# Kernel tuning notes

Measured on AMD Instinct MI355X. Metric: run time of the kernel, lower is better.

Reference implementation:

```python
import jax, jax.numpy as jnp
import numpy as np

N = 100000          # nodes
E = 800000          # edges per relation
R = 6               # relations
B = 1000            # graphs
IN_DIM = 14
POS_COL = 5
PE = 8              # pos_emb_dim
H = 128             # hidden_dim
OUT = 128           # out_dim
NPOS = 24
D1 = IN_DIM - 1 + PE  # 21, GAT layer-1 input dim


def setup_inputs() -> dict:
    key = jax.random.key(0)
    ks = jax.random.split(key, 20)
    x_all = jax.random.normal(ks[0], (N, IN_DIM), dtype=jnp.float32)
    pos = jax.random.randint(ks[1], (N,), 0, NPOS)
    x_all = x_all.at[:, POS_COL].set(pos.astype(jnp.float32))
    edges = jax.random.randint(ks[2], (R, 2, E), 0, N, dtype=jnp.int32)
    batch = jnp.sort(jax.random.randint(ks[3], (N,), 0, B, dtype=jnp.int32))
    pos_table = jax.random.normal(ks[4], (NPOS, PE), dtype=jnp.float32) * 0.02
    W1 = jax.random.normal(ks[5], (R, D1, H), dtype=jnp.float32) * 0.1
    as1 = jax.random.normal(ks[6], (R, H), dtype=jnp.float32) * 0.1
    ad1 = jax.random.normal(ks[7], (R, H), dtype=jnp.float32) * 0.1
    b1 = jnp.zeros((R, H), dtype=jnp.float32)
    W2 = jax.random.normal(ks[8], (R, H, H), dtype=jnp.float32) * 0.05
    as2 = jax.random.normal(ks[9], (R, H), dtype=jnp.float32) * 0.1
    ad2 = jax.random.normal(ks[10], (R, H), dtype=jnp.float32) * 0.1
    b2 = jnp.zeros((R, H), dtype=jnp.float32)
    n1w = jnp.ones((H,), dtype=jnp.float32)
    n1b = jnp.zeros((H,), dtype=jnp.float32)
    n2w = jnp.ones((H,), dtype=jnp.float32)
    n2b = jnp.zeros((H,), dtype=jnp.float32)
    query = jax.random.normal(ks[11], (H,), dtype=jnp.float32) * 0.02
    projW = jax.random.normal(ks[12], (H, OUT), dtype=jnp.float32) * 0.05
    projb = jnp.zeros((OUT,), dtype=jnp.float32)
    return dict(x_all=x_all, edges=edges, batch=batch, pos_table=pos_table,
                W1=W1, as1=as1, ad1=ad1, b1=b1, W2=W2, as2=as2, ad2=ad2, b2=b2,
                n1w=n1w, n1b=n1b, n2w=n2w, n2b=n2b, query=query, projW=projW, projb=projb)


def _seg_softmax(logits, seg, num):
    m = jax.lax.stop_gradient(jax.ops.segment_max(logits, seg, num_segments=num))
    e = jnp.exp(logits - m[seg])
    s = jax.ops.segment_sum(e, seg, num_segments=num)
    return e / s[seg]


def _gat_layer(x, W, a_s, a_d, b, edges):
    # sum over R relation-specific GATConv(heads=1, concat=False) outputs
    n = x.shape[0]
    out = jnp.zeros((n, W.shape[-1]), dtype=x.dtype)
    for r in range(R):
        xp = x @ W[r]                       # [N, H] projected features
        src, dst = edges[r, 0], edges[r, 1]
        z = (xp @ a_s[r])[src] + (xp @ a_d[r])[dst]
        z = jnp.where(z > 0, z, 0.2 * z)    # LeakyReLU(0.2)
        alpha = _seg_softmax(z, dst, n)     # per-destination softmax
        agg = jax.ops.segment_sum(alpha[:, None] * xp[src], dst, num_segments=n)
        out = out + agg + b[r]
    return out


def _ln(x, w, b):
    mu = x.mean(-1, keepdims=True)
    v = ((x - mu) ** 2).mean(-1, keepdims=True)
    return (x - mu) / jnp.sqrt(v + 1e-5) * w + b


def reference(x_all, edges, batch, pos_table, W1, as1, ad1, b1,
              W2, as2, ad2, b2, n1w, n1b, n2w, n2b, query, projW, projb):
    cont = jnp.concatenate([x_all[:, :POS_COL], x_all[:, POS_COL + 1:]], axis=1)
    pidx = jnp.clip(x_all[:, POS_COL].astype(jnp.int32), 0, NPOS - 1)
    x = jnp.concatenate([cont, pos_table[pidx]], axis=1)  # [N, D1]
    x = _gat_layer(x, W1, as1, ad1, b1, edges)
    x = _ln(jax.nn.gelu(x, approximate=False), n1w, n1b)
    x = _gat_layer(x, W2, as2, ad2, b2, edges)
    x = _ln(jax.nn.gelu(x, approximate=False), n2w, n2b)
    # AttentionPooling: gather-score-softmax-scatter over batch segments
    scores = x @ query
    w = _seg_softmax(scores, batch, B)
    pool = jax.ops.segment_sum(w[:, None] * x, batch, num_segments=B)  # [B, H]
    return pool @ projW + projb
```

## Files before the change

### kernel.cpp

```cpp
#include <hip/hip_runtime.h>
#include <math.h>

#define NN   100000
#define EE   800000
#define RR   6
#define BB   1000
#define HH   128
#define MM   (RR*NN)
#define NBPR ((NN + 255) >> 8)
#define NBK  (RR * NBPR)
#define CH   4096
#define CAP  4096

static inline int ceil_div(int a, int b){ return (a+b-1)/b; }

typedef __attribute__((ext_vector_type(8))) short bf16x8;
typedef __attribute__((ext_vector_type(4))) short bf16x4;
typedef __attribute__((ext_vector_type(4))) float f32x4;

__device__ __forceinline__ unsigned fenc(float f){
  unsigned u = __float_as_uint(f);
  return (u & 0x80000000u) ? ~u : (u | 0x80000000u);
}
__device__ __forceinline__ float fdec(unsigned u){
  return __uint_as_float((u & 0x80000000u) ? (u & 0x7fffffffu) : ~u);
}
__device__ __forceinline__ unsigned short f2bf(float f){
  unsigned u = __float_as_uint(f);
  return (unsigned short)((u + 0x7fffu + ((u >> 16) & 1u)) >> 16);
}
__device__ __forceinline__ float bf2f(unsigned short h){
  return __uint_as_float(((unsigned)h) << 16);
}

__global__ void k_binscatter(const int* __restrict__ edges, int* __restrict__ bcur,
                             unsigned* __restrict__ ebkt)
{
  __shared__ int hist[NBPR];
  __shared__ int base[NBPR];
  int t = threadIdx.x;
  const int nch = (EE + CH - 1) / CH;
  int r = blockIdx.x / nch, c = blockIdx.x - r*nch;
  for (int i = t; i < NBPR; i += 256) hist[i] = 0;
  __syncthreads();
  const int* sptr = edges + (size_t)r*2*EE;
  const int* dptr = sptr + EE;
  int e0 = c*CH, e1 = min(EE, e0 + CH);
  for (int i = e0 + t; i < e1; i += 256)
    atomicAdd(&hist[dptr[i] >> 8], 1);
  __syncthreads();
  for (int i = t; i < NBPR; i += 256) {
    int h = hist[i];
    int gb = r*NBPR + i;
    base[i] = h ? (gb*CAP + atomicAdd(&bcur[gb], h)) : 0;
    hist[i] = 0;
  }
  __syncthreads();
  for (int i = e0 + t; i < e1; i += 256) {
    int dst = dptr[i];
    int b = dst >> 8;
    int slot = base[b] + atomicAdd(&hist[b], 1);
    ebkt[slot] = ((unsigned)sptr[i] << 8) | (unsigned)(dst & 255);
  }
}

__global__ void k_bscan(const int* __restrict__ bcur, int* __restrict__ boff,
                        int* __restrict__ off)
{
  __shared__ int sh[256];
  int t = threadIdx.x;
  int carry = 0;
  for (int c = 0; c < NBK; c += 256) {
    int idx = c + t;
    int v = (idx < NBK) ? bcur[idx] : 0;
    sh[t] = v;
    __syncthreads();
    for (int o = 1; o < 256; o <<= 1) {
      int add = (t >= o) ? sh[t-o] : 0;
      __syncthreads();
      sh[t] += add;
      __syncthreads();
    }
    int incl = sh[t];
    int tot  = sh[255];
    if (idx < NBK) boff[idx] = carry + incl - v;
    __syncthreads();
    carry += tot;
  }
  if (t == 0) { boff[NBK] = carry; off[MM] = carry; }
}

__global__ void k_bbuild(const unsigned* __restrict__ ebkt, const int* __restrict__ bcur,
                         const int* __restrict__ boff,
                         int* __restrict__ off, int* __restrict__ elist)
{
  __shared__ int cnt[256];
  __shared__ int sc[256];
  __shared__ int cur[256];
  int t = threadIdx.x;
  int bb = blockIdx.x;
  int e0r = bb*CAP, e1r = e0r + bcur[bb];
  int w0 = boff[bb];
  cnt[t] = 0;
  __syncthreads();
  for (int i = e0r + t; i < e1r; i += 256)
    atomicAdd(&cnt[ebkt[i] & 255u], 1);
  __syncthreads();
  sc[t] = cnt[t];
  __syncthreads();
  for (int o = 1; o < 256; o <<= 1) {
    int add = (t >= o) ? sc[t-o] : 0;
    __syncthreads();
    sc[t] += add;
    __syncthreads();
  }
  int excl = sc[t] - cnt[t];
  int r = bb / NBPR, b = bb - r*NBPR;
  int dst = b*256 + t;
  if (dst < NN) off[r*NN + dst] = w0 + excl;
  cur[t] = w0 + excl;
  __syncthreads();
  for (int i = e0r + t; i < e1r; i += 256) {
    unsigned w = ebkt[i];
    int slot = atomicAdd(&cur[w & 255u], 1);
    elist[slot] = (int)(w >> 8);
  }
}

__global__ void k_featprep(const float* __restrict__ x_all, const float* __restrict__ pos_table,
                           short* __restrict__ x0h, short* __restrict__ x0l)
{
  int gid = blockIdx.x*256 + threadIdx.x;
  if (gid >= NN*32) return;
  int nidx = gid >> 5, c = gid & 31;
  float v = 0.f;
  if (c < 13) {
    int scl = (c < 5) ? c : c + 1;
    v = x_all[nidx*14 + scl];
  } else if (c < 21) {
    int pi = (int)x_all[nidx*14 + 5];
    pi = pi < 0 ? 0 : (pi > 23 ? 23 : pi);
    v = pos_table[pi*8 + (c - 13)];
  }
  unsigned short h = f2bf(v);
  unsigned short l = f2bf(v - bf2f(h));
  x0h[gid] = (short)h;
  x0l[gid] = (short)l;
}

template<int KP>
__global__ void k_wprep(const float* __restrict__ W, int K,
                        short* __restrict__ Wh, short* __restrict__ Wl)
{
  int gid = blockIdx.x*256 + threadIdx.x;
  if (gid >= RR*128*KP) return;
  int r = gid / (128*KP);
  int rem = gid - r*(128*KP);
  int nn = rem / KP, k = rem - nn*KP;
  float v = (k < K) ? W[((size_t)r*K + k)*128 + nn] : 0.f;
  unsigned short h = f2bf(v);
  unsigned short l = f2bf(v - bf2f(h));
  Wh[gid] = (short)h;
  Wl[gid] = (short)l;
}

template<int KP>
__global__ void k_wa(const float* __restrict__ W, const float* __restrict__ as,
                     const float* __restrict__ ad, int K, float* __restrict__ wa)
{
  int idx = blockIdx.x*256 + threadIdx.x;
  if (idx >= 12*KP) return;
  int rr = idx / KP, k = idx - rr*KP;
  int r = (rr < 6) ? rr : rr - 6;
  const float* a = ((rr < 6) ? as : ad) + (size_t)r*HH;
  float s = 0.f;
  if (k < K) {
    const float* wrow = W + ((size_t)r*K + k)*128;
    #pragma unroll 8
    for (int h = 0; h < 128; ++h) s = fmaf(wrow[h], a[h], s);
  }
  wa[idx] = s;
}

__global__ void k_zsd32(const short* __restrict__ xh, const short* __restrict__ xl,
                        const float* __restrict__ wa, float* __restrict__ zsd, int n)
{
  __shared__ float w[12*32];
  int tid = threadIdx.x;
  for (int i = tid; i < 12*32; i += 256) w[i] = wa[i];
  __syncthreads();
  int g = blockIdx.x*256 + tid;
  if (g >= n) return;
  float v[32];
  #pragma unroll
  for (int c = 0; c < 4; ++c) {
    uint4 vh = *(const uint4*)(xh + (size_t)g*32 + c*8);
    uint4 vl = *(const uint4*)(xl + (size_t)g*32 + c*8);
    const unsigned short* hp = (const unsigned short*)&vh;
    const unsigned short* lp = (const unsigned short*)&vl;
    #pragma unroll
    for (int j = 0; j < 8; ++j) v[c*8+j] = bf2f(hp[j]) + bf2f(lp[j]);
  }
  #pragma unroll
  for (int rr = 0; rr < 12; ++rr) {
    float d = 0.f;
    #pragma unroll
    for (int k = 0; k < 32; ++k) d = fmaf(v[k], w[rr*32+k], d);
    zsd[(size_t)rr*n + g] = d;
  }
}

__global__ void k_agg1(const unsigned short* __restrict__ x0h, const float* __restrict__ zsd,
                       const int* __restrict__ elist, const int* __restrict__ off,
                       unsigned short* __restrict__ aggH, unsigned short* __restrict__ aggL,
                       int n)
{
  int gid = blockIdx.x*256 + threadIdx.x;
  int g = gid >> 4;
  int l = threadIdx.x & 15;
  if (g >= n) return;
  int sub = l >> 2, ch = l & 3;

  for (int rel = 0; rel < RR; ++rel) {
    const float* zsr = zsd + (size_t)rel*n;
    const float* zdr = zsd + (size_t)(6+rel)*n;
    int o0 = off[(size_t)rel*NN + g];
    int deg = off[(size_t)rel*NN + g + 1] - o0;
    float acc[8] = {0,0,0,0,0,0,0,0};
    float inv = 0.f;
    if (deg > 0) {
      float zdd = zdr[g];
      float m = -3.4e38f, es = 0.f;
      for (int i = l; i < deg; i += 16) {
        float z = zsr[elist[o0+i]] + zdd;
        z = (z > 0.f) ? z : 0.2f*z;
        float mn = fmaxf(m, z);
        es = es*__expf(m - mn) + __expf(z - mn);
        m = mn;
      }
      #pragma unroll
      for (int o = 1; o <= 8; o <<= 1) {
        float mo = __shfl_xor(m, o), eo = __shfl_xor(es, o);
        float mn = fmaxf(m, mo);
        es = es*__expf(m - mn) + eo*__expf(mo - mn);
        m = mn;
      }
      inv = 1.f / es;
      for (int base = 0; base < deg; base += 4) {
        int i = base + sub;
        float ew = 0.f; int ss = 0;
        if (i < deg) {
          ss = elist[o0+i];
          float z = zsr[ss] + zdd;
          z = (z > 0.f) ? z : 0.2f*z;
          ew = __expf(z - m);
        }
        uint4 v = *(const uint4*)(x0h + (size_t)ss*32 + ch*8);
        acc[0] = fmaf(ew, __uint_as_float(v.x << 16),         acc[0]);
        acc[1] = fmaf(ew, __uint_as_float(v.x & 0xffff0000u), acc[1]);
        acc[2] = fmaf(ew, __uint_as_float(v.y << 16),         acc[2]);
        acc[3] = fmaf(ew, __uint_as_float(v.y & 0xffff0000u), acc[3]);
        acc[4] = fmaf(ew, __uint_as_float(v.z << 16),         acc[4]);
        acc[5] = fmaf(ew, __uint_as_float(v.z & 0xffff0000u), acc[5]);
        acc[6] = fmaf(ew, __uint_as_float(v.w << 16),         acc[6]);
        acc[7] = fmaf(ew, __uint_as_float(v.w & 0xffff0000u), acc[7]);
      }
      #pragma unroll
      for (int j = 0; j < 8; ++j) {
        acc[j] += __shfl_xor(acc[j], 4);
        acc[j] += __shfl_xor(acc[j], 8);
      }
    }
    if (sub == 0) {
      uint4 ph, pl;
      unsigned* php = (unsigned*)&ph; unsigned* plp = (unsigned*)&pl;
      #pragma unroll
      for (int j2 = 0; j2 < 4; ++j2) {
        float a0 = acc[2*j2]   * inv;
        float a1 = acc[2*j2+1] * inv;
        unsigned short h0 = f2bf(a0), h1 = f2bf(a1);
        php[j2] = ((unsigned)h1 << 16) | h0;
        plp[j2] = ((unsigned)f2bf(a1 - bf2f(h1)) << 16) | f2bf(a0 - bf2f(h0));
      }
      size_t o = ((size_t)rel*n + g)*32 + ch*8;
      *(uint4*)(aggH + o) = ph;
      *(uint4*)(aggL + o) = pl;
    }
  }
}

__device__ __forceinline__ bf16x8 ldfragG(const short* __restrict__ p, int row, int kb, int KP_)
{
  bf16x4 a = *(const bf16x4*)(p + (size_t)row*KP_ + kb);
  bf16x4 b = *(const bf16x4*)(p + (size_t)row*KP_ + kb + 16);
  return __builtin_shufflevector(a, b, 0,1,2,3,4,5,6,7);
}

__global__ __launch_bounds__(256, 4)
void k_gemm1(const short* __restrict__ aggH, const short* __restrict__ aggL,
             const short* __restrict__ Wh, const short* __restrict__ Wl,
             const float* __restrict__ bsv,
             const float* __restrict__ nw, const float* __restrict__ nb,
             unsigned short* __restrict__ Yh, unsigned short* __restrict__ Yl, int n)
{
  __shared__ __align__(16) float Cs[32*136];
  int tid = threadIdx.x;
  int r0 = blockIdx.x * 32;
  int wid = tid >> 6, lane = tid & 63;
  int lr = lane & 15, lg = lane >> 4;
  int rt = wid >> 1;
  int c0 = (wid & 1) * 4;
  int arow = r0 + rt*16 + lr;
  int kb = 4*lg;
  f32x4 acct[4] = {{0,0,0,0},{0,0,0,0},{0,0,0,0},{0,0,0,0}};

  for (int rel = 0; rel < RR; ++rel) {
    const short* Ahr = aggH + (size_t)rel*n*32;
    const short* Alr = aggL + (size_t)rel*n*32;
    const short* Whr = Wh + (size_t)rel*128*32;
    const short* Wlr = Wl + (size_t)rel*128*32;
    bf16x8 ah = ldfragG(Ahr, arow, kb, 32);
    bf16x8 al = ldfragG(Alr, arow, kb, 32);
    #pragma unroll
    for (int t = 0; t < 4; ++t) {
      int wrow = (c0 + t)*16 + lr;
      bf16x8 whf = ldfragG(Whr, wrow, kb, 32);
      bf16x8 wlf = ldfragG(Wlr, wrow, kb, 32);
      acct[t] = __builtin_amdgcn_mfma_f32_16x16x32_bf16(ah, whf, acct[t], 0, 0, 0);
      acct[t] = __builtin_amdgcn_mfma_f32_16x16x32_bf16(al, whf, acct[t], 0, 0, 0);
      acct[t] = __builtin_amdgcn_mfma_f32_16x16x32_bf16(ah, wlf, acct[t], 0, 0, 0);
    }
  }

  #pragma unroll
  for (int t = 0; t < 4; ++t)
    #pragma unroll
    for (int v = 0; v < 4; ++v) {
      int row = rt*16 + lg*4 + v;
      int col = (c0 + t)*16 + lr;
      float x = acct[t][v] + bsv[col];
      Cs[row*136 + col] = 0.5f*x*(1.f + erff(x*0.70710678118654752f));
    }
  __syncthreads();
  {
    int r = tid >> 3, sg = tid & 7;
    float vals[16];
    float s = 0.f;
    #pragma unroll
    for (int i = 0; i < 16; ++i) { vals[i] = Cs[r*136 + sg*16 + i]; s += vals[i]; }
    s += __shfl_xor(s, 1); s += __shfl_xor(s, 2); s += __shfl_xor(s, 4);
    float mu = s * (1.f/128.f);
    float var = 0.f;
    #pragma unroll
    for (int i = 0; i < 16; ++i) { vals[i] -= mu; var += vals[i]*vals[i]; }
    var += __shfl_xor(var, 1); var += __shfl_xor(var, 2); var += __shfl_xor(var, 4);
    float inv = 1.f / sqrtf(var*(1.f/128.f) + 1e-5f);
    int g = r0 + r;
    uint4 ph0, ph1, pl0, pl1;
    unsigned* php0 = (unsigned*)&ph0; unsigned* php1 = (unsigned*)&ph1;
    unsigned* plp0 = (unsigned*)&pl0; unsigned* plp1 = (unsigned*)&pl1;
    #pragma unroll
    for (int j2 = 0; j2 < 8; ++j2) {
      int c = sg*16 + 2*j2;
      float y0 = vals[2*j2]  *inv*nw[c]   + nb[c];
      float y1 = vals[2*j2+1]*inv*nw[c+1] + nb[c+1];
      unsigned short h0 = f2bf(y0), h1 = f2bf(y1);
      unsigned hw = ((unsigned)h1 << 16) | h0;
      unsigned lw = ((unsigned)f2bf(y1 - bf2f(h1)) << 16) | f2bf(y0 - bf2f(h0));
      if (j2 < 4) { php0[j2] = hw; plp0[j2] = lw; }
      else        { php1[j2-4] = hw; plp1[j2-4] = lw; }
    }
    *(uint4*)(Yh + (size_t)g*128 + sg*16)     = ph0;
    *(uint4*)(Yh + (size_t)g*128 + sg*16 + 8) = ph1;
    *(uint4*)(Yl + (size_t)g*128 + sg*16)     = pl0;
    *(uint4*)(Yl + (size_t)g*128 + sg*16 + 8) = pl1;
  }
}

__device__ __forceinline__ bf16x8 ldfrag_(const short* p, int row, int kb, int KP_, int smask)
{
  int xr = row & smask;
  int s0 = (((kb)      >> 3) ^ xr) * 8 + (kb & 7);
  int s1 = (((kb + 16) >> 3) ^ xr) * 8 + (kb & 7);
  bf16x4 a = *(const bf16x4*)(p + (size_t)row*KP_ + s0);
  bf16x4 b = *(const bf16x4*)(p + (size_t)row*KP_ + s1);
  return __builtin_shufflevector(a, b, 0,1,2,3,4,5,6,7);
}

template<int KP>
__global__ __launch_bounds__(256, 2)
void k_gemm_mfma(const short* __restrict__ Ah, const short* __restrict__ Al,
                 const short* __restrict__ WhAll, const short* __restrict__ WlAll,
                 const float* __restrict__ a_sAll, const float* __restrict__ a_dAll,
                 unsigned short* __restrict__ xpbAll, float* __restrict__ zsAll,
                 float* __restrict__ zdAll, int rbase, int n)
{
  constexpr int SLOTS = KP/8;
  constexpr int SMASK = (SLOTS >= 8) ? 7 : (SLOTS-1);
  __shared__ short lds[320*KP];
  constexpr int AH0 = 0, AL0 = 32*KP, WH0 = 64*KP, WL0 = 192*KP;
  int tid = threadIdx.x;
  int r0 = blockIdx.x * 32;
  int ry = blockIdx.y;
  const short* Wh = WhAll + (size_t)(rbase+ry)*128*KP;
  const short* Wl = WlAll + (size_t)(rbase+ry)*128*KP;
  const float* a_s = a_sAll + (size_t)(rbase+ry)*HH;
  const float* a_d = a_dAll + (size_t)(rbase+ry)*HH;
  unsigned short* xpb = xpbAll + (size_t)ry*n*128;
  float* zs = zsAll + (size_t)ry*n;
  float* zd = zdAll + (size_t)ry*n;

  for (int ch = tid; ch < 32*SLOTS; ch += 256) {
    int row = ch / SLOTS, slot = ch - row*SLOTS;
    int gr = r0 + row;
    int dsl = (slot ^ (row & SMASK)) * 8;
    bf16x8 vh, vl;
    if (gr < n) {
      vh = *(const bf16x8*)(Ah + (size_t)gr*KP + slot*8);
      vl = *(const bf16x8*)(Al + (size_t)gr*KP + slot*8);
    } else {
      #pragma unroll
      for (int q = 0; q < 8; ++q) { vh[q] = 0; vl[q] = 0; }
    }
    *(bf16x8*)(lds + AH0 + row*KP + dsl) = vh;
    *(bf16x8*)(lds + AL0 + row*KP + dsl) = vl;
  }
  for (int ch = tid; ch < 128*SLOTS; ch += 256) {
    int row = ch / SLOTS, slot = ch - row*SLOTS;
    int dsl = (slot ^ (row & SMASK)) * 8;
    *(bf16x8*)(lds + WH0 + row*KP + dsl) = *(const bf16x8*)(Wh + (size_t)row*KP + slot*8);
    *(bf16x8*)(lds + WL0 + row*KP + dsl) = *(const bf16x8*)(Wl + (size_t)row*KP + slot*8);
  }
  __syncthreads();

  int wid = tid >> 6, lane = tid & 63;
  int lr = lane & 15, lg = lane >> 4;
  int rt = wid >> 1;
  int c0 = (wid & 1) * 4;
  f32x4 acc[4] = {{0,0,0,0},{0,0,0,0},{0,0,0,0},{0,0,0,0}};
  int arow = rt*16 + lr;

  #pragma unroll
  for (int kc = 0; kc < KP/32; ++kc) {
    int kb = kc*32 + 4*lg;
    bf16x8 ah = ldfrag_(lds + AH0, arow, kb, KP, SMASK);
    bf16x8 al = ldfrag_(lds + AL0, arow, kb, KP, SMASK);
    #pragma unroll
    for (int t = 0; t < 4; ++t) {
      int wrow = (c0 + t)*16 + lr;
      bf16x8 wh = ldfrag_(lds + WH0, wrow, kb, KP, SMASK);
      bf16x8 wl = ldfrag_(lds + WL0, wrow, kb, KP, SMASK);
      acc[t] = __builtin_amdgcn_mfma_f32_16x16x32_bf16(ah, wh, acc[t], 0, 0, 0);
      acc[t] = __builtin_amdgcn_mfma_f32_16x16x32_bf16(ah, wl, acc[t], 0, 0, 0);
      acc[t] = __builtin_amdgcn_mfma_f32_16x16x32_bf16(al, wh, acc[t], 0, 0, 0);
    }
  }
  __syncthreads();

  float* Cs = (float*)lds;
  #pragma unroll
  for (int t = 0; t < 4; ++t)
    #pragma unroll
    for (int v = 0; v < 4; ++v) {
      int row = rt*16 + lg*4 + v;
      int col = (c0 + t)*16 + lr;
      Cs[row*136 + col] = acc[t][v];
    }
  __syncthreads();

  {
    int r = tid >> 3, sg = tid & 7;
    float ps = 0.f, pd = 0.f;
    #pragma unroll
    for (int i = 0; i < 16; ++i) {
      int c = sg*16 + i;
      float x = Cs[r*136 + c];
      ps = fmaf(x, a_s[c], ps);
      pd = fmaf(x, a_d[c], pd);
    }
    ps += __shfl_xor(ps, 1); pd += __shfl_xor(pd, 1);
    ps += __shfl_xor(ps, 2); pd += __shfl_xor(pd, 2);
    ps += __shfl_xor(ps, 4); pd += __shfl_xor(pd, 4);
    int gr = r0 + r;
    if (sg == 0 && gr < n) { zs[gr] = ps; zd[gr] = pd; }
  }
  for (int i = tid; i < 32*16; i += 256) {
    int row = i >> 4, q = i & 15;
    int gr = r0 + row;
    if (gr < n) {
      const float* cp = Cs + row*136 + q*8;
      uint4 o;
      o.x = ((unsigned)f2bf(cp[1]) << 16) | f2bf(cp[0]);
      o.y = ((unsigned)f2bf(cp[3]) << 16) | f2bf(cp[2]);
      o.z = ((unsigned)f2bf(cp[5]) << 16) | f2bf(cp[4]);
      o.w = ((unsigned)f2bf(cp[7]) << 16) | f2bf(cp[6]);
      *(uint4*)(xpb + (size_t)gr*128 + q*8) = o;
    }
  }
}

template<int NREL, int FIN>
__global__ void k_agg3(const unsigned short* __restrict__ xpb,
                       const float* __restrict__ zs,
                       const float* __restrict__ zd,
                       const int* __restrict__ elist,
                       const int* __restrict__ off,
                       float* __restrict__ hacc,
                       const float* __restrict__ bsum,
                       const float* __restrict__ nw, const float* __restrict__ nb,
                       float* __restrict__ Yf,
                       const float* __restrict__ q,
                       const int* __restrict__ batch,
                       float* __restrict__ scores, unsigned* __restrict__ bmax,
                       int n)
{
  int gid = blockIdx.x*256 + threadIdx.x;
  int g = gid >> 4;
  int l = threadIdx.x & 15;
  int gbase = threadIdx.x & 48;
  if (g >= n) return;

  float acc[8] = {0,0,0,0,0,0,0,0};

  #pragma unroll
  for (int r = 0; r < NREL; ++r) {
    int o0 = off[(size_t)r*NN + g], o1 = off[(size_t)r*NN + g + 1];
    int deg = o1 - o0;
    if (deg <= 0) continue;
    const float* zsr = zs + (size_t)r*n;
    float zdd = zd[(size_t)r*n + g];

    float m = -3.4e38f;
    for (int i = l; i < deg; i += 16) {
      float z = zsr[elist[o0+i]] + zdd;
      z = (z > 0.f) ? z : 0.2f*z;
      m = fmaxf(m, z);
    }
    m = fmaxf(m, __shfl_xor(m, 1));
    m = fmaxf(m, __shfl_xor(m, 2));
    m = fmaxf(m, __shfl_xor(m, 4));
    m = fmaxf(m, __shfl_xor(m, 8));

    float tmp[8] = {0,0,0,0,0,0,0,0};
    float esum = 0.f;
    const unsigned short* xr = xpb + (size_t)r*n*128;
    for (int base = 0; base < deg; base += 16) {
      int i = base + l;
      float ew = 0.f; int s = 0;
      if (i < deg) {
        s = elist[o0+i];
        float z = zsr[s] + zdd;
        z = (z > 0.f) ? z : 0.2f*z;
        ew = __expf(z - m);
      }
      esum += ew;
      int cnt = min(16, deg - base);
      for (int t = 0; t < cnt; ++t) {
        float w = __shfl(ew, gbase + t);
        int ss = __shfl(s, gbase + t);
        const uint4 v = *(const uint4*)(xr + (size_t)ss*128 + l*8);
        tmp[0] = fmaf(w, __uint_as_float(v.x << 16),          tmp[0]);
        tmp[1] = fmaf(w, __uint_as_float(v.x & 0xffff0000u),  tmp[1]);
        tmp[2] = fmaf(w, __uint_as_float(v.y << 16),          tmp[2]);
        tmp[3] = fmaf(w, __uint_as_float(v.y & 0xffff0000u),  tmp[3]);
        tmp[4] = fmaf(w, __uint_as_float(v.z << 16),          tmp[4]);
        tmp[5] = fmaf(w, __uint_as_float(v.z & 0xffff0000u),  tmp[5]);
        tmp[6] = fmaf(w, __uint_as_float(v.w << 16),          tmp[6]);
        tmp[7] = fmaf(w, __uint_as_float(v.w & 0xffff0000u),  tmp[7]);
      }
    }
    esum += __shfl_xor(esum, 1);
    esum += __shfl_xor(esum, 2);
    esum += __shfl_xor(esum, 4);
    esum += __shfl_xor(esum, 8);
    float inv = 1.f / esum;
    #pragma unroll
    for (int j = 0; j < 8; ++j) acc[j] = fmaf(tmp[j], inv, acc[j]);
  }

  if (FIN == 0) {
    float* hp = hacc + (size_t)g*128 + l*8;
    float4 o0; o0.x = acc[0]; o0.y = acc[1]; o0.z = acc[2]; o0.w = acc[3];
    float4 o1; o1.x = acc[4]; o1.y = acc[5]; o1.z = acc[6]; o1.w = acc[7];
    *(float4*)hp = o0;
    *(float4*)(hp + 4) = o1;
  } else {
    if (FIN == 2) {
      const float* hp = hacc + (size_t)g*128 + l*8;
      float4 p0 = *(const float4*)hp;
      float4 p1 = *(const float4*)(hp + 4);
      acc[0] += p0.x; acc[1] += p0.y; acc[2] += p0.z; acc[3] += p0.w;
      acc[4] += p1.x; acc[5] += p1.y; acc[6] += p1.z; acc[7] += p1.w;
    }
    float4 b0 = *(const float4*)(bsum + l*8);
    float4 b1 = *(const float4*)(bsum + l*8 + 4);
    acc[0] += b0.x; acc[1] += b0.y; acc[2] += b0.z; acc[3] += b0.w;
    acc[4] += b1.x; acc[5] += b1.y; acc[6] += b1.z; acc[7] += b1.w;
    float s = 0.f;
    #pragma unroll
    for (int j = 0; j < 8; ++j) {
      acc[j] = 0.5f*acc[j]*(1.f + erff(acc[j]*0.70710678118654752f));
      s += acc[j];
    }
    s += __shfl_xor(s, 1); s += __shfl_xor(s, 2);
    s += __shfl_xor(s, 4); s += __shfl_xor(s, 8);
    float mu = s * (1.f/128.f);
    float v = 0.f;
    #pragma unroll
    for (int j = 0; j < 8; ++j) { acc[j] -= mu; v += acc[j]*acc[j]; }
    v += __shfl_xor(v, 1); v += __shfl_xor(v, 2);
    v += __shfl_xor(v, 4); v += __shfl_xor(v, 8);
    v *= (1.f/128.f);
    float inv = 1.f / sqrtf(v + 1e-5f);
    float4 w0 = *(const float4*)(nw + l*8);
    float4 w1 = *(const float4*)(nw + l*8 + 4);
    float4 nb0 = *(const float4*)(nb + l*8);
    float4 nb1 = *(const float4*)(nb + l*8 + 4);
    float y[8];
    y[0] = acc[0]*inv*w0.x + nb0.x; y[1] = acc[1]*inv*w0.y + nb0.y;
    y[2] = acc[2]*inv*w0.z + nb0.z; y[3] = acc[3]*inv*w0.w + nb0.w;
    y[4] = acc[4]*inv*w1.x + nb1.x; y[5] = acc[5]*inv*w1.y + nb1.y;
    y[6] = acc[6]*inv*w1.z + nb1.z; y[7] = acc[7]*inv*w1.w + nb1.w;
    float* yp = Yf + (size_t)g*128 + l*8;
    float4 o0; o0.x = y[0]; o0.y = y[1]; o0.z = y[2]; o0.w = y[3];
    float4 o1; o1.x = y[4]; o1.y = y[5]; o1.z = y[6]; o1.w = y[7];
    *(float4*)yp = o0;
    *(float4*)(yp + 4) = o1;
    float4 q0 = *(const float4*)(q + l*8);
    float4 q1 = *(const float4*)(q + l*8 + 4);
    float sc = y[0]*q0.x + y[1]*q0.y + y[2]*q0.z + y[3]*q0.w
             + y[4]*q1.x + y[5]*q1.y + y[6]*q1.z + y[7]*q1.w;
    sc += __shfl_xor(sc, 1); sc += __shfl_xor(sc, 2);
    sc += __shfl_xor(sc, 4); sc += __shfl_xor(sc, 8);
    if (l == 0) {
      scores[g] = sc;
      atomicMax(&bmax[batch[g]], fenc(sc));
    }
  }
}

__global__ void k_bsum(const float* __restrict__ b, float* __restrict__ bs)
{
  int t = threadIdx.x;
  float s = 0.f;
  #pragma unroll
  for (int r = 0; r < RR; ++r) s += b[r*HH + t];
  bs[t] = s;
}

__global__ void k_segbounds(const int* __restrict__ batch, int* __restrict__ segst,
                            int n, int numB)
{
  int b = blockIdx.x*256 + threadIdx.x;
  if (b > numB) return;
  int lo = 0, hi = n;
  while (lo < hi) { int mid = (lo+hi) >> 1; if (batch[mid] < b) lo = mid+1; else hi = mid; }
  segst[b] = lo;
}

__global__ void k_pool(const float* __restrict__ X, const float* __restrict__ scores,
                       const int* __restrict__ segst, const unsigned* __restrict__ bmax,
                       float* __restrict__ pool, int numB)
{
  int b = blockIdx.x;
  int t = threadIdx.x;
  int s0 = segst[b], s1 = segst[b+1];
  float m = fdec(bmax[b]);
  float acc0 = 0.f, acc1 = 0.f, esum = 0.f;
  int i = s0;
  for (; i + 1 < s1; i += 2) {
    float e0 = __expf(scores[i] - m);
    float e1 = __expf(scores[i+1] - m);
    esum += e0 + e1;
    acc0 = fmaf(e0, X[(size_t)i*128 + t], acc0);
    acc1 = fmaf(e1, X[(size_t)(i+1)*128 + t], acc1);
  }
  if (i < s1) {
    float e0 = __expf(scores[i] - m);
    esum += e0;
    acc0 = fmaf(e0, X[(size_t)i*128 + t], acc0);
  }
  float inv = (s1 > s0) ? 1.f/esum : 0.f;
  pool[(size_t)b*128 + t] = (acc0 + acc1) * inv;
}

__global__ void k_outgemm(const float* __restrict__ pool, const float* __restrict__ projW,
                          const float* __restrict__ projb, float* __restrict__ out, int numB)
{
  int b = blockIdx.x;
  int j = threadIdx.x;
  __shared__ float p[128];
  p[j] = pool[(size_t)b*128 + j];
  __syncthreads();
  float acc = projb[j];
  #pragma unroll 16
  for (int k = 0; k < 128; ++k) acc = fmaf(p[k], projW[(size_t)k*128 + j], acc);
  out[(size_t)b*128 + j] = acc;
}

extern "C" void kernel_launch(void* const* d_in, const int* in_sizes, int n_in,
                              void* d_out, int out_size, void* d_ws, size_t ws_size,
                              hipStream_t stream)
{
  const float* x_all = (const float*)d_in[0];
  const int*   edges = (const int*)d_in[1];
  const int*   batch = (const int*)d_in[2];
  const float* pos_table = (const float*)d_in[3];
  const float* W1  = (const float*)d_in[4];
  const float* as1 = (const float*)d_in[5];
  const float* ad1 = (const float*)d_in[6];
  const float* b1  = (const float*)d_in[7];
  const float* W2  = (const float*)d_in[8];
  const float* as2 = (const float*)d_in[9];
  const float* ad2 = (const float*)d_in[10];
  const float* b2  = (const float*)d_in[11];
  const float* n1w = (const float*)d_in[12];
  const float* n1b = (const float*)d_in[13];
  const float* n2w = (const float*)d_in[14];
  const float* n2b = (const float*)d_in[15];
  const float* query = (const float*)d_in[16];
  const float* projW = (const float*)d_in[17];
  const float* projb = (const float*)d_in[18];
  float* out = (float*)d_out;
  (void)in_sizes; (void)n_in; (void)out_size;

  const bool use6 = ws_size >= ((size_t)300 << 20);

  char* p = (char*)d_ws;
  auto alloc = [&](size_t b){ void* r = (void*)p; p += (b + 255) & ~(size_t)255; return r; };
  int*   off   = (int*)alloc((size_t)(MM+1)*sizeof(int));
  int*   elist = (int*)alloc((size_t)RR*EE*sizeof(int));
  int*   boff  = (int*)alloc((size_t)(NBK+1)*sizeof(int));
  int*   bcur  = (int*)alloc((size_t)NBK*sizeof(int));
  short* wtH   = (short*)alloc((size_t)RR*128*128*sizeof(short));
  short* wtL   = (short*)alloc((size_t)RR*128*128*sizeof(short));
  float* wa    = (float*)alloc((size_t)12*128*sizeof(float));
  float* zsd   = (float*)alloc((size_t)12*NN*sizeof(float));
  float* bsv   = (float*)alloc(128*sizeof(float));
  int*   segst = (int*)alloc((size_t)(BB+1)*sizeof(int));
  unsigned* bmax = (unsigned*)alloc((size_t)BB*sizeof(unsigned));
  float* pool  = (float*)alloc((size_t)BB*HH*sizeof(float));
  float* scrs  = (float*)alloc((size_t)NN*sizeof(float));
  size_t xpbRel = use6 ? 6 : 3;
  unsigned short* xpb = (unsigned short*)alloc((size_t)xpbRel*NN*128*sizeof(short));
  float* R1    = (float*)alloc((size_t)NN*128*sizeof(float));
  float* R2    = (float*)alloc((size_t)NN*128*sizeof(float));

  unsigned* ebkt = (unsigned*)R1;
  short* x0h = (short*)R1;
  short* x0l = x0h + (size_t)NN*32;
  float* hacc = R1;
  unsigned short* h1h = (unsigned short*)R2;
  unsigned short* h1l = h1h + (size_t)NN*128;
  float* h2 = use6 ? R1 : R2;
  unsigned short* aggH = (unsigned short*)xpb;
  unsigned short* aggL = aggH + (size_t)RR*NN*32;
  float* zs = zsd;
  float* zd = zsd + (use6 ? (size_t)6*NN : (size_t)3*NN);

  const int nch = (EE + CH - 1) / CH;
  hipMemsetAsync(bcur, 0, (size_t)NBK*sizeof(int), stream);
  k_binscatter<<<RR*nch,256,0,stream>>>(edges, bcur, ebkt);
  k_bscan<<<1,256,0,stream>>>(bcur, boff, off);
  k_bbuild<<<NBK,256,0,stream>>>(ebkt, bcur, boff, off, elist);

  k_featprep<<<ceil_div(NN*32,256),256,0,stream>>>(x_all, pos_table, x0h, x0l);
  k_segbounds<<<ceil_div(BB+1,256),256,0,stream>>>(batch, segst, NN, BB);
  hipMemsetAsync(bmax, 0, (size_t)BB*sizeof(unsigned), stream);

  k_wa<32><<<ceil_div(12*32,256),256,0,stream>>>(W1, as1, ad1, 21, wa);
  k_zsd32<<<ceil_div(NN,256),256,0,stream>>>(x0h, x0l, wa, zsd, NN);
  k_wprep<32><<<ceil_div(RR*128*32,256),256,0,stream>>>(W1, 21, wtH, wtL);
  k_bsum<<<1,128,0,stream>>>(b1, bsv);
  k_agg1<<<ceil_div(NN*16,256),256,0,stream>>>((const unsigned short*)x0h, zsd, elist, off,
                                               aggH, aggL, NN);
  k_gemm1<<<ceil_div(NN,32),256,0,stream>>>((const short*)aggH, (const short*)aggL,
                                            wtH, wtL, bsv, n1w, n1b, h1h, h1l, NN);

  k_wprep<128><<<ceil_div(RR*128*128,256),256,0,stream>>>(W2, 128, wtH, wtL);
  k_bsum<<<1,128,0,stream>>>(b2, bsv);
  int aggGrid = ceil_div(NN*16, 256);
  if (use6) {
    dim3 g6(ceil_div(NN,32), 6);
    k_gemm_mfma<128><<<g6,256,0,stream>>>((const short*)h1h, (const short*)h1l,
                                          wtH, wtL, as2, ad2, xpb, zs, zd, 0, NN);
    k_agg3<6,3><<<aggGrid,256,0,stream>>>(xpb, zs, zd, elist, off, (float*)0,
        bsv, n2w, n2b, h2, query, batch, scrs, bmax, NN);
  } else {
    dim3 g3(ceil_div(NN,32), 3);
    k_gemm_mfma<128><<<g3,256,0,stream>>>((const short*)h1h, (const short*)h1l,
                                          wtH, wtL, as2, ad2, xpb, zs, zd, 0, NN);
    k_agg3<3,0><<<aggGrid,256,0,stream>>>(xpb, zs, zd, elist, off, hacc,
        bsv, n2w, n2b, (float*)0, query, batch, scrs, bmax, NN);
    k_gemm_mfma<128><<<g3,256,0,stream>>>((const short*)h1h, (const short*)h1l,
                                          wtH, wtL, as2, ad2, xpb, zs, zd, 3, NN);
    k_agg3<3,2><<<aggGrid,256,0,stream>>>(xpb, zs, zd, elist, off + (size_t)3*NN, hacc,
        bsv, n2w, n2b, h2, query, batch, scrs, bmax, NN);
  }

  k_pool<<<BB,128,0,stream>>>(h2, scrs, segst, bmax, pool, BB);
  k_outgemm<<<BB,128,0,stream>>>(pool, projW, projb, out, BB);
}
```

Before: 912.2 us.

## Drop low-bf16 half of hidden activations, unroll gathers, size workspace exactly

Result: faster. 872.4 us (-4.4%).

```diff
diff --git a/kernel.cpp b/kernel.cpp
--- a/kernel.cpp
+++ b/kernel.cpp
@@ -246,24 +246,39 @@
         m = mn;
       }
       inv = 1.f / es;
-      for (int base = 0; base < deg; base += 4) {
-        int i = base + sub;
-        float ew = 0.f; int ss = 0;
-        if (i < deg) {
-          ss = elist[o0+i];
-          float z = zsr[ss] + zdd;
+      for (int base = 0; base < deg; base += 8) {
+        int i0 = base + sub, i1 = base + 4 + sub;
+        float e0 = 0.f, e1 = 0.f; int s0 = 0, s1 = 0;
+        if (i0 < deg) {
+          s0 = elist[o0+i0];
+          float z = zsr[s0] + zdd;
           z = (z > 0.f) ? z : 0.2f*z;
-          ew = __expf(z - m);
+          e0 = __expf(z - m);
         }
-        uint4 v = *(const uint4*)(x0h + (size_t)ss*32 + ch*8);
-        acc[0] = fmaf(ew, __uint_as_float(v.x << 16),         acc[0]);
-        acc[1] = fmaf(ew, __uint_as_float(v.x & 0xffff0000u), acc[1]);
-        acc[2] = fmaf(ew, __uint_as_float(v.y << 16),         acc[2]);
-        acc[3] = fmaf(ew, __uint_as_float(v.y & 0xffff0000u), acc[3]);
-        acc[4] = fmaf(ew, __uint_as_float(v.z << 16),         acc[4]);
-        acc[5] = fmaf(ew, __uint_as_float(v.z & 0xffff0000u), acc[5]);
-        acc[6] = fmaf(ew, __uint_as_float(v.w << 16),         acc[6]);
-        acc[7] = fmaf(ew, __uint_as_float(v.w & 0xffff0000u), acc[7]);
+        if (i1 < deg) {
+          s1 = elist[o0+i1];
+          float z = zsr[s1] + zdd;
+          z = (z > 0.f) ? z : 0.2f*z;
+          e1 = __expf(z - m);
+        }
+        uint4 v0 = *(const uint4*)(x0h + (size_t)s0*32 + ch*8);
+        uint4 v1 = *(const uint4*)(x0h + (size_t)s1*32 + ch*8);
+        acc[0] = fmaf(e0, __uint_as_float(v0.x << 16),         acc[0]);
+        acc[1] = fmaf(e0, __uint_as_float(v0.x & 0xffff0000u), acc[1]);
+        acc[2] = fmaf(e0, __uint_as_float(v0.y << 16),         acc[2]);
+        acc[3] = fmaf(e0, __uint_as_float(v0.y & 0xffff0000u), acc[3]);
+        acc[4] = fmaf(e0, __uint_as_float(v0.z << 16),         acc[4]);
+        acc[5] = fmaf(e0, __uint_as_float(v0.z & 0xffff0000u), acc[5]);
+        acc[6] = fmaf(e0, __uint_as_float(v0.w << 16),         acc[6]);
+        acc[7] = fmaf(e0, __uint_as_float(v0.w & 0xffff0000u), acc[7]);
+        acc[0] = fmaf(e1, __uint_as_float(v1.x << 16),         acc[0]);
+        acc[1] = fmaf(e1, __uint_as_float(v1.x & 0xffff0000u), acc[1]);
+        acc[2] = fmaf(e1, __uint_as_float(v1.y << 16),         acc[2]);
+        acc[3] = fmaf(e1, __uint_as_float(v1.y & 0xffff0000u), acc[3]);
+        acc[4] = fmaf(e1, __uint_as_float(v1.z << 16),         acc[4]);
+        acc[5] = fmaf(e1, __uint_as_float(v1.z & 0xffff0000u), acc[5]);
+        acc[6] = fmaf(e1, __uint_as_float(v1.w << 16),         acc[6]);
+        acc[7] = fmaf(e1, __uint_as_float(v1.w & 0xffff0000u), acc[7]);
       }
       #pragma unroll
       for (int j = 0; j < 8; ++j) {
@@ -301,7 +316,7 @@
              const short* __restrict__ Wh, const short* __restrict__ Wl,
              const float* __restrict__ bsv,
              const float* __restrict__ nw, const float* __restrict__ nb,
-             unsigned short* __restrict__ Yh, unsigned short* __restrict__ Yl, int n)
+             unsigned short* __restrict__ Yh, int n)
 {
   __shared__ __align__(16) float Cs[32*136];
   int tid = threadIdx.x;
@@ -356,24 +371,18 @@
     var += __shfl_xor(var, 1); var += __shfl_xor(var, 2); var += __shfl_xor(var, 4);
     float inv = 1.f / sqrtf(var*(1.f/128.f) + 1e-5f);
     int g = r0 + r;
-    uint4 ph0, ph1, pl0, pl1;
+    uint4 ph0, ph1;
     unsigned* php0 = (unsigned*)&ph0; unsigned* php1 = (unsigned*)&ph1;
-    unsigned* plp0 = (unsigned*)&pl0; unsigned* plp1 = (unsigned*)&pl1;
     #pragma unroll
     for (int j2 = 0; j2 < 8; ++j2) {
       int c = sg*16 + 2*j2;
       float y0 = vals[2*j2]  *inv*nw[c]   + nb[c];
       float y1 = vals[2*j2+1]*inv*nw[c+1] + nb[c+1];
-      unsigned short h0 = f2bf(y0), h1 = f2bf(y1);
-      unsigned hw = ((unsigned)h1 << 16) | h0;
-      unsigned lw = ((unsigned)f2bf(y1 - bf2f(h1)) << 16) | f2bf(y0 - bf2f(h0));
-      if (j2 < 4) { php0[j2] = hw; plp0[j2] = lw; }
-      else        { php1[j2-4] = hw; plp1[j2-4] = lw; }
+      unsigned hw = ((unsigned)f2bf(y1) << 16) | f2bf(y0);
+      if (j2 < 4) php0[j2] = hw; else php1[j2-4] = hw;
     }
     *(uint4*)(Yh + (size_t)g*128 + sg*16)     = ph0;
     *(uint4*)(Yh + (size_t)g*128 + sg*16 + 8) = ph1;
-    *(uint4*)(Yl + (size_t)g*128 + sg*16)     = pl0;
-    *(uint4*)(Yl + (size_t)g*128 + sg*16 + 8) = pl1;
   }
 }
 
@@ -389,7 +398,7 @@
 
 template<int KP>
 __global__ __launch_bounds__(256, 2)
-void k_gemm_mfma(const short* __restrict__ Ah, const short* __restrict__ Al,
+void k_gemm_mfma(const short* __restrict__ Ah,
                  const short* __restrict__ WhAll, const short* __restrict__ WlAll,
                  const float* __restrict__ a_sAll, const float* __restrict__ a_dAll,
                  unsigned short* __restrict__ xpbAll, float* __restrict__ zsAll,
@@ -397,8 +406,8 @@
 {
   constexpr int SLOTS = KP/8;
   constexpr int SMASK = (SLOTS >= 8) ? 7 : (SLOTS-1);
-  __shared__ short lds[320*KP];
-  constexpr int AH0 = 0, AL0 = 32*KP, WH0 = 64*KP, WL0 = 192*KP;
+  __shared__ short lds[288*KP];
+  constexpr int AH0 = 0, WH0 = 32*KP, WL0 = 160*KP;
   int tid = threadIdx.x;
   int r0 = blockIdx.x * 32;
   int ry = blockIdx.y;
@@ -414,16 +423,14 @@
     int row = ch / SLOTS, slot = ch - row*SLOTS;
     int gr = r0 + row;
     int dsl = (slot ^ (row & SMASK)) * 8;
-    bf16x8 vh, vl;
+    bf16x8 vh;
     if (gr < n) {
       vh = *(const bf16x8*)(Ah + (size_t)gr*KP + slot*8);
-      vl = *(const bf16x8*)(Al + (size_t)gr*KP + slot*8);
     } else {
       #pragma unroll
-      for (int q = 0; q < 8; ++q) { vh[q] = 0; vl[q] = 0; }
+      for (int q = 0; q < 8; ++q) vh[q] = 0;
     }
     *(bf16x8*)(lds + AH0 + row*KP + dsl) = vh;
-    *(bf16x8*)(lds + AL0 + row*KP + dsl) = vl;
   }
   for (int ch = tid; ch < 128*SLOTS; ch += 256) {
     int row = ch / SLOTS, slot = ch - row*SLOTS;
@@ -444,7 +451,6 @@
   for (int kc = 0; kc < KP/32; ++kc) {
     int kb = kc*32 + 4*lg;
     bf16x8 ah = ldfrag_(lds + AH0, arow, kb, KP, SMASK);
-    bf16x8 al = ldfrag_(lds + AL0, arow, kb, KP, SMASK);
     #pragma unroll
     for (int t = 0; t < 4; ++t) {
       int wrow = (c0 + t)*16 + lr;
@@ -452,7 +458,6 @@
       bf16x8 wl = ldfrag_(lds + WL0, wrow, kb, KP, SMASK);
       acc[t] = __builtin_amdgcn_mfma_f32_16x16x32_bf16(ah, wh, acc[t], 0, 0, 0);
       acc[t] = __builtin_amdgcn_mfma_f32_16x16x32_bf16(ah, wl, acc[t], 0, 0, 0);
-      acc[t] = __builtin_amdgcn_mfma_f32_16x16x32_bf16(al, wh, acc[t], 0, 0, 0);
     }
   }
   __syncthreads();
@@ -498,6 +503,16 @@
     }
   }
 }
+
+#define ACC8(W_, U_) \
+  tmp[0] = fmaf(W_, __uint_as_float((U_).x << 16),         tmp[0]); \
+  tmp[1] = fmaf(W_, __uint_as_float((U_).x & 0xffff0000u), tmp[1]); \
+  tmp[2] = fmaf(W_, __uint_as_float((U_).y << 16),         tmp[2]); \
+  tmp[3] = fmaf(W_, __uint_as_float((U_).y & 0xffff0000u), tmp[3]); \
+  tmp[4] = fmaf(W_, __uint_as_float((U_).z << 16),         tmp[4]); \
+  tmp[5] = fmaf(W_, __uint_as_float((U_).z & 0xffff0000u), tmp[5]); \
+  tmp[6] = fmaf(W_, __uint_as_float((U_).w << 16),         tmp[6]); \
+  tmp[7] = fmaf(W_, __uint_as_float((U_).w & 0xffff0000u), tmp[7]);
 
 template<int NREL, int FIN>
 __global__ void k_agg3(const unsigned short* __restrict__ xpb,
@@ -522,7 +537,6 @@
 
   float acc[8] = {0,0,0,0,0,0,0,0};
 
-  #pragma unroll
   for (int r = 0; r < NREL; ++r) {
     int o0 = off[(size_t)r*NN + g], o1 = off[(size_t)r*NN + g + 1];
     int deg = o1 - o0;
@@ -555,18 +569,23 @@
       }
       esum += ew;
       int cnt = min(16, deg - base);
-      for (int t = 0; t < cnt; ++t) {
-        float w = __shfl(ew, gbase + t);
-        int ss = __shfl(s, gbase + t);
-        const uint4 v = *(const uint4*)(xr + (size_t)ss*128 + l*8);
-        tmp[0] = fmaf(w, __uint_as_float(v.x << 16),          tmp[0]);
-        tmp[1] = fmaf(w, __uint_as_float(v.x & 0xffff0000u),  tmp[1]);
-        tmp[2] = fmaf(w, __uint_as_float(v.y << 16),          tmp[2]);
-        tmp[3] = fmaf(w, __uint_as_float(v.y & 0xffff0000u),  tmp[3]);
-        tmp[4] = fmaf(w, __uint_as_float(v.z << 16),          tmp[4]);
-        tmp[5] = fmaf(w, __uint_as_float(v.z & 0xffff0000u),  tmp[5]);
-        tmp[6] = fmaf(w, __uint_as_float(v.w << 16),          tmp[6]);
-        tmp[7] = fmaf(w, __uint_as_float(v.w & 0xffff0000u),  tmp[7]);
+      for (int t = 0; t < cnt; t += 4) {
+        float w0 = __shfl(ew, gbase + t);
+        float w1 = __shfl(ew, gbase + t + 1);
+        float w2 = __shfl(ew, gbase + t + 2);
+        float w3 = __shfl(ew, gbase + t + 3);
+        int a0 = __shfl(s, gbase + t);
+        int a1 = __shfl(s, gbase + t + 1);
+        int a2 = __shfl(s, gbase + t + 2);
+        int a3 = __shfl(s, gbase + t + 3);
+        uint4 u0 = *(const uint4*)(xr + (size_t)a0*128 + l*8);
+        uint4 u1 = *(const uint4*)(xr + (size_t)a1*128 + l*8);
+        uint4 u2 = *(const uint4*)(xr + (size_t)a2*128 + l*8);
+        uint4 u3 = *(const uint4*)(xr + (size_t)a3*128 + l*8);
+        ACC8(w0, u0);
+        ACC8(w1, u1);
+        ACC8(w2, u2);
+        ACC8(w3, u3);
       }
     }
     esum += __shfl_xor(esum, 1);
@@ -724,7 +743,15 @@
   float* out = (float*)d_out;
   (void)in_sizes; (void)n_in; (void)out_size;
 
-  const bool use6 = ws_size >= ((size_t)300 << 20);
+  auto asz = [](size_t b){ return (b + 255) & ~(size_t)255; };
+  size_t baseNeed =
+      asz((size_t)(MM+1)*4) + asz((size_t)RR*EE*4) + asz((size_t)(NBK+1)*4) +
+      asz((size_t)NBK*4) + 2*asz((size_t)RR*128*128*2) + asz((size_t)12*128*4) +
+      asz((size_t)12*NN*4) + asz(128*4) + asz((size_t)(BB+1)*4) + asz((size_t)BB*4) +
+      asz((size_t)BB*HH*4) + asz((size_t)NN*4) +
+      asz((size_t)NN*128*4)  + asz((size_t)NN*128*4) ;
+  size_t need6 = baseNeed + asz((size_t)6*NN*128*2);
+  const bool use6 = ws_size >= need6;
 
   char* p = (char*)d_ws;
   auto alloc = [&](size_t b){ void* r = (void*)p; p += (b + 255) & ~(size_t)255; return r; };
@@ -751,8 +778,7 @@
   short* x0l = x0h + (size_t)NN*32;
   float* hacc = R1;
   unsigned short* h1h = (unsigned short*)R2;
-  unsigned short* h1l = h1h + (size_t)NN*128;
-  float* h2 = use6 ? R1 : R2;
+  float* h2 = (float*)R2;
   unsigned short* aggH = (unsigned short*)xpb;
   unsigned short* aggL = aggH + (size_t)RR*NN*32;
   float* zs = zsd;
@@ -775,24 +801,24 @@
   k_agg1<<<ceil_div(NN*16,256),256,0,stream>>>((const unsigned short*)x0h, zsd, elist, off,
                                                aggH, aggL, NN);
   k_gemm1<<<ceil_div(NN,32),256,0,stream>>>((const short*)aggH, (const short*)aggL,
-                                            wtH, wtL, bsv, n1w, n1b, h1h, h1l, NN);
+                                            wtH, wtL, bsv, n1w, n1b, h1h, NN);
 
   k_wprep<128><<<ceil_div(RR*128*128,256),256,0,stream>>>(W2, 128, wtH, wtL);
   k_bsum<<<1,128,0,stream>>>(b2, bsv);
   int aggGrid = ceil_div(NN*16, 256);
   if (use6) {
     dim3 g6(ceil_div(NN,32), 6);
-    k_gemm_mfma<128><<<g6,256,0,stream>>>((const short*)h1h, (const short*)h1l,
+    k_gemm_mfma<128><<<g6,256,0,stream>>>((const short*)h1h,
                                           wtH, wtL, as2, ad2, xpb, zs, zd, 0, NN);
     k_agg3<6,3><<<aggGrid,256,0,stream>>>(xpb, zs, zd, elist, off, (float*)0,
         bsv, n2w, n2b, h2, query, batch, scrs, bmax, NN);
   } else {
     dim3 g3(ceil_div(NN,32), 3);
-    k_gemm_mfma<128><<<g3,256,0,stream>>>((const short*)h1h, (const short*)h1l,
+    k_gemm_mfma<128><<<g3,256,0,stream>>>((const short*)h1h,
                                           wtH, wtL, as2, ad2, xpb, zs, zd, 0, NN);
     k_agg3<3,0><<<aggGrid,256,0,stream>>>(xpb, zs, zd, elist, off, hacc,
         bsv, n2w, n2b, (float*)0, query, batch, scrs, bmax, NN);
-    k_gemm_mfma<128><<<g3,256,0,stream>>>((const short*)h1h, (const short*)h1l,
+    k_gemm_mfma<128><<<g3,256,0,stream>>>((const short*)h1h,
                                           wtH, wtL, as2, ad2, xpb, zs, zd, 3, NN);
     k_agg3<3,2><<<aggGrid,256,0,stream>>>(xpb, zs, zd, elist, off + (size_t)3*NN, hacc,
         bsv, n2w, n2b, h2, query, batch, scrs, bmax, NN);
```
